# Optimization experiments

Hardware: AMD Instinct MI355X
Metric: run time of the kernel (lower is better)

## Reference

```python
import jax, jax.numpy as jnp
import numpy as np
from jax import lax

PC_RANGE = (-51.2, -51.2, -3.0, 51.2, 51.2, 1.0)
VOXEL = (0.4, 0.4, 4.0)
H = 256
W = 256
C = 256
EPS = 1e-5


def setup_inputs() -> dict:
    key = jax.random.key(0)
    ks = jax.random.split(key, 12)
    B, N = 4, 32
    # boxes: centers inside the BEV range with small corner offsets
    centers = jax.random.uniform(ks[0], (B, N, 1, 2), minval=-45.0, maxval=45.0)
    offsets = jax.random.normal(ks[1], (B, N, 8, 2)) * 2.0
    z = jax.random.normal(ks[2], (B, N, 8, 1))
    pred_box = jnp.concatenate([centers + offsets, z], axis=-1).astype(jnp.float32)
    pred_score = jax.random.uniform(ks[3], (B, N), dtype=jnp.float32)
    s = 0.02
    return {
        "pred_box": pred_box,
        "pred_score": pred_score,
        "W1": jax.random.normal(ks[4], (25, C), dtype=jnp.float32) * s,
        "b1": jnp.zeros((C,), jnp.float32),
        "W2": jax.random.normal(ks[5], (C, C), dtype=jnp.float32) * s,
        "b2": jnp.zeros((C,), jnp.float32),
        "W3": jax.random.normal(ks[6], (C, C), dtype=jnp.float32) * s,
        "b3": jnp.zeros((C,), jnp.float32),
        "conv_w": jax.random.normal(ks[7], (3, 2, C, C, 3, 3), dtype=jnp.float32) * s,
        "gamma": jnp.ones((3, 2, C), jnp.float32),
        "beta": jnp.zeros((3, 2, C), jnp.float32),
    }


def _conv(x, w):
    # x: [B,C,H,W], w: [O,I,3,3]
    return lax.conv_general_dilated(x, w, (1, 1), "SAME",
                                    dimension_numbers=("NCHW", "OIHW", "NCHW"))


def _bn(x, g, b):
    # BatchNorm2d in training mode; original runs with batch size 1 per CAV,
    # so stats are per-sample over (H,W). x: [B,C,H,W]
    m = x.mean(axis=(2, 3), keepdims=True)
    v = ((x - m) ** 2).mean(axis=(2, 3), keepdims=True)
    return (x - m) * jax.lax.rsqrt(v + EPS) * g[None, :, None, None] + b[None, :, None, None]


def reference(pred_box, pred_score, W1, b1, W2, b2, W3, b3, conv_w, gamma, beta):
    B, N = pred_box.shape[:2]
    xmin, ymin, _, xmax, ymax, _ = PC_RANGE
    dx, dy, _ = VOXEL

    # per-box MLP embedding
    geom = pred_box.reshape(B, N, 24)
    obj = jnp.concatenate([geom, pred_score[..., None]], axis=-1)  # [B,N,25]
    h1 = jax.nn.relu(obj @ W1 + b1)
    h2 = jax.nn.relu(h1 @ W2 + b2)
    obj_feat = (h2 @ W3 + b3) * pred_score[..., None]  # [B,N,C]

    # rasterize box AABBs onto the grid; later boxes overwrite earlier ones
    corners = pred_box[..., :2]  # [B,N,8,2]
    gx = jnp.floor((corners[..., 0] - xmin) / dx)
    gy = jnp.floor((corners[..., 1] - ymin) / dy)
    gx0 = jnp.clip(gx.min(-1), 0, W - 1).astype(jnp.int32)  # [B,N]
    gx1 = jnp.clip(gx.max(-1), 0, W - 1).astype(jnp.int32)
    gy0 = jnp.clip(gy.min(-1), 0, H - 1).astype(jnp.int32)
    gy1 = jnp.clip(gy.max(-1), 0, H - 1).astype(jnp.int32)

    xs = jnp.arange(W)
    ys = jnp.arange(H)
    mx = (xs[None, None, :] >= gx0[..., None]) & (xs[None, None, :] <= gx1[..., None])  # [B,N,W]
    my = (ys[None, None, :] >= gy0[..., None]) & (ys[None, None, :] <= gy1[..., None])  # [B,N,H]
    cover = my[:, :, :, None] & mx[:, :, None, :]  # [B,N,H,W]

    prio = jnp.arange(N, dtype=jnp.int32)[None, :, None, None]
    last = jnp.max(jnp.where(cover, prio, -1), axis=1)  # [B,H,W]: index of last covering box
    idx = jnp.clip(last, 0)
    gathered = jax.vmap(lambda of, ix: of[ix])(obj_feat, idx)  # [B,H,W,C]
    feat = jnp.where(last[..., None] >= 0, gathered, 0.0)
    x = jnp.transpose(feat, (0, 3, 1, 2))  # [B,C,H,W]

    # residual conv refine blocks
    for k in range(3):
        res = x
        y = jax.nn.relu(_bn(_conv(x, conv_w[k, 0]), gamma[k, 0], beta[k, 0]))
        y = _bn(_conv(y, conv_w[k, 1]), gamma[k, 1], beta[k, 1])
        x = jax.nn.relu(y + res)
    return x
```

## Files before the change

### kernel.cpp

```cpp
#include <hip/hip_runtime.h>
#include <hip/hip_bf16.h>

typedef short short8 __attribute__((ext_vector_type(8)));
typedef float f32x16 __attribute__((ext_vector_type(16)));

#define MFMA32 __builtin_amdgcn_mfma_f32_32x32x16_bf16
#define HWPX 65536

#define GLDS16(gp, lp) __builtin_amdgcn_global_load_lds( \
    (const __attribute__((address_space(1))) unsigned int*)(gp), \
    (__attribute__((address_space(3))) unsigned int*)(lp), 16, 0, 0)

__device__ __forceinline__ unsigned short f2bf(float f) {
  unsigned u = __float_as_uint(f);
  u += 0x7FFF + ((u >> 16) & 1);
  return (unsigned short)(u >> 16);
}
__device__ __forceinline__ float bf2f(unsigned short b) {
  return __uint_as_float(((unsigned)b) << 16);
}

__global__ void mlp_kernel(const float* __restrict__ pred_box,
                           const float* __restrict__ score,
                           const float* __restrict__ W1, const float* __restrict__ b1,
                           const float* __restrict__ W2, const float* __restrict__ b2,
                           const float* __restrict__ W3, const float* __restrict__ b3,
                           float* __restrict__ objf) {
  __shared__ float obj[25];
  __shared__ float h1[256];
  __shared__ float h2[256];
  const int box = blockIdx.x;
  const int tid = threadIdx.x;
  if (tid < 24) obj[tid] = pred_box[box * 24 + tid];
  if (tid == 24) obj[24] = score[box];
  __syncthreads();
  float acc = b1[tid];
  #pragma unroll
  for (int k = 0; k < 25; ++k) acc = fmaf(obj[k], W1[k * 256 + tid], acc);
  h1[tid] = fmaxf(acc, 0.f);
  __syncthreads();
  acc = b2[tid];
  #pragma unroll 8
  for (int k = 0; k < 256; ++k) acc = fmaf(h1[k], W2[k * 256 + tid], acc);
  h2[tid] = fmaxf(acc, 0.f);
  __syncthreads();
  acc = b3[tid];
  #pragma unroll 8
  for (int k = 0; k < 256; ++k) acc = fmaf(h2[k], W3[k * 256 + tid], acc);
  objf[box * 256 + tid] = acc * score[box];
}

__global__ void bounds_kernel(const float* __restrict__ pred_box,
                              int* __restrict__ bnds) {
  const int t = threadIdx.x;
  const float* p = pred_box + t * 24;
  float gx0 = 1e30f, gx1 = -1e30f, gy0 = 1e30f, gy1 = -1e30f;
  #pragma unroll
  for (int j = 0; j < 8; ++j) {
    float gx = floorf((p[j * 3 + 0] + 51.2f) / 0.4f);
    float gy = floorf((p[j * 3 + 1] + 51.2f) / 0.4f);
    gx0 = fminf(gx0, gx); gx1 = fmaxf(gx1, gx);
    gy0 = fminf(gy0, gy); gy1 = fmaxf(gy1, gy);
  }
  bnds[t * 4 + 0] = (int)fminf(fmaxf(gx0, 0.f), 255.f);
  bnds[t * 4 + 1] = (int)fminf(fmaxf(gx1, 0.f), 255.f);
  bnds[t * 4 + 2] = (int)fminf(fmaxf(gy0, 0.f), 255.f);
  bnds[t * 4 + 3] = (int)fminf(fmaxf(gy1, 0.f), 255.f);
}

__global__ void wt_kernel(const float* __restrict__ w, unsigned short* __restrict__ wt) {
  int i = blockIdx.x * 256 + threadIdx.x;
  int j = i & 7;
  int l = (i >> 3) & 63;
  int nb = (i >> 9) & 7;
  int ks = (i >> 12) & 15;
  int t2 = i >> 16;
  int tap = t2 % 9;
  int cv = t2 / 9;
  int co = nb * 32 + (l & 31);
  int ci = ks * 16 + ((l >> 5) << 3) + j;
  wt[i] = f2bf(w[(size_t)((cv * 256 + co) * 256 + ci) * 9 + tap]);
}

__global__ void raster_nhwc(const int* __restrict__ bnds,
                            const float* __restrict__ objf,
                            unsigned short* __restrict__ xB) {
  const int y = blockIdx.x;
  const int b = blockIdx.y;
  const int x = threadIdx.x;
  __shared__ int sb[128];
  __shared__ int lastA[256];
  if (x < 128) sb[x] = bnds[b * 128 + x];
  __syncthreads();
  int last = -1;
  #pragma unroll
  for (int n = 0; n < 32; ++n) {
    int bx0 = sb[n * 4 + 0], bx1 = sb[n * 4 + 1];
    int by0 = sb[n * 4 + 2], by1 = sb[n * 4 + 3];
    if (x >= bx0 && x <= bx1 && y >= by0 && y <= by1) last = n;
  }
  lastA[x] = last;
  __syncthreads();
  unsigned short* row = xB + ((size_t)b * HWPX + y * 256) * 256;
  for (int it = 0; it < 32; ++it) {
    int s = x + 256 * it;
    int px = s >> 5;
    int c8 = (s & 31) * 8;
    int ln = lastA[px];
    short8 v = {0, 0, 0, 0, 0, 0, 0, 0};
    if (ln >= 0) {
      const float* f = objf + (b * 32 + ln) * 256 + c8;
      #pragma unroll
      for (int j = 0; j < 8; ++j) v[j] = (short)f2bf(f[j]);
    }
    *(short8*)(row + px * 256 + c8) = v;
  }
}

__global__ __launch_bounds__(256, 2) void conv_mfma(const unsigned short* __restrict__ in,
                                                    const unsigned short* __restrict__ wt,
                                                    const unsigned short* __restrict__ zbuf,
                                                    unsigned short* __restrict__ T,
                                                    float* __restrict__ part) {
  __shared__ unsigned short lds[2][16 * 528];
  const int bid0 = blockIdx.x;
  const int swz = (bid0 & 7) * 256 + (bid0 >> 3);
  const int b = swz >> 9;
  const int bid = swz & 511;
  const int x0 = (bid & 3) * 64;
  const int y0 = (bid >> 2) * 2;
  const int tid = threadIdx.x;
  const int lane = tid & 63;
  const int wid = tid >> 6;
  const int h = lane >> 5;
  const int l31 = lane & 31;
  const int col0 = l31 * 8;

  const unsigned short* inb = in + (size_t)b * (HWPX * 256);
  unsigned short* Tb = T + (size_t)b * (HWPX * 256);

  f32x16 acc[4][2];
  #pragma unroll
  for (int a = 0; a < 4; ++a)
    #pragma unroll
    for (int n = 0; n < 2; ++n)
      #pragma unroll
      for (int r = 0; r < 16; ++r) acc[a][n][r] = 0.f;

  const unsigned short* wbase = wt + (size_t)(wid * 2) * 512 + lane * 8;

  short8 edgev;

  auto stage = [&](int c1, int buf) {
    const int ci0 = c1 * 32;
    #pragma unroll
    for (int i = 0; i < 4; ++i) {
      const int rowg = wid * 4 + i;
      const int row = rowg >> 2;
      const int g = rowg & 3;
      const int yg = y0 + row - 1;
      unsigned short* lp = &lds[buf][((row << 2) | ((g & 1) << 1) | (g >> 1)) * 528 + 8];
      const unsigned short* gp;
      if ((unsigned)yg < 256u)
        gp = inb + ((size_t)(yg * 256 + x0 + lane) * 256 + ci0 + g * 8);
      else
        gp = zbuf + lane * 8;
      GLDS16(gp, lp);
    }
  };

  auto edge_load = [&](int c1) {
    edgev = (short8){0, 0, 0, 0, 0, 0, 0, 0};
    if (tid < 32) {
      int row = tid >> 3, side = (tid >> 2) & 1, g = tid & 3;
      int yg = y0 + row - 1;
      int xg = x0 + (side ? 64 : -1);
      if ((unsigned)yg < 256u && (unsigned)xg < 256u)
        edgev = *(const short8*)(inb + ((size_t)(yg * 256 + xg) * 256 + c1 * 32 + g * 8));
    }
  };
  auto edge_store = [&](int buf) {
    if (tid < 32) {
      int row = tid >> 3, side = (tid >> 2) & 1, g = tid & 3;
      *(short8*)&lds[buf][((row << 2) | ((g & 1) << 1) | (g >> 1)) * 528 + (side ? 65 : 0) * 8] = edgev;
    }
  };

  #define LOADA(s, d) { \
    const int ks_ = (s) / 9, tap_ = (s) % 9, ky_ = tap_ / 3, kx_ = tap_ % 3; \
    const unsigned short* p_ = lbase + ky_ * 2112 + ks_ * 528 + kx_ * 8 + col0; \
    d[0] = *(const short8*)(p_); \
    d[1] = *(const short8*)(p_ + 256); \
    d[2] = *(const short8*)(p_ + 2112); \
    d[3] = *(const short8*)(p_ + 2368); }

  #define LOADB(s, d) { \
    const unsigned short* p_ = wbase + (size_t)((((s) % 9) * 16 + c * 2 + (s) / 9) * 8) * 512; \
    d[0] = *(const short8*)(p_); d[1] = *(const short8*)(p_ + 512); }

  auto compute = [&](int buf, int c) {
    const unsigned short* lbase = &lds[buf][h * 1056];
    short8 Af[2][4];
    short8 Bf[3][2];
    LOADA(0, Af[0]);
    LOADB(0, Bf[0]);
    LOADB(1, Bf[1]);
    #pragma unroll
    for (int s = 0; s < 18; ++s) {
      if (s + 2 < 18) LOADB(s + 2, Bf[(s + 2) % 3]);
      if (s + 1 < 18) LOADA(s + 1, Af[(s + 1) & 1]);
      __builtin_amdgcn_s_setprio(1);
      #pragma unroll
      for (int mf = 0; mf < 4; ++mf)
        #pragma unroll
        for (int nf = 0; nf < 2; ++nf)
          acc[mf][nf] = MFMA32(Af[s & 1][mf], Bf[s % 3][nf], acc[mf][nf], 0, 0, 0);
      __builtin_amdgcn_s_setprio(0);
    }
  };

  stage(0, 0);
  edge_load(0);
  edge_store(0);
  asm volatile("s_waitcnt lgkmcnt(0)" ::: "memory");

  int cur = 0;
  for (int c = 0; c < 8; ++c) {
    if (c < 7) {
      stage(c + 1, cur ^ 1);
      asm volatile("s_waitcnt vmcnt(8)" ::: "memory");
    } else {
      asm volatile("s_waitcnt vmcnt(0)" ::: "memory");
    }
    __builtin_amdgcn_s_barrier();
    if (c < 7) edge_load(c + 1);
    compute(cur, c);
    if (c < 7) edge_store(cur ^ 1);
    asm volatile("s_waitcnt lgkmcnt(0)" ::: "memory");
    __builtin_amdgcn_s_barrier();
    cur ^= 1;
  }

  #pragma unroll
  for (int mf = 0; mf < 4; ++mf)
    #pragma unroll
    for (int nf = 0; nf < 2; ++nf) {
      unsigned short* o = Tb + ((size_t)((y0 + (mf >> 1)) * 256) + x0 + (mf & 1) * 32) * 256
                          + wid * 64 + nf * 32 + l31;
      #pragma unroll
      for (int r = 0; r < 16; ++r) {
        int m = (r & 3) + 8 * (r >> 2) + 4 * h;
        o[(size_t)m * 256] = f2bf(acc[mf][nf][r]);
      }
    }
  #pragma unroll
  for (int nf = 0; nf < 2; ++nf) {
    float s = 0.f, s2 = 0.f;
    #pragma unroll
    for (int mf = 0; mf < 4; ++mf)
      #pragma unroll
      for (int r = 0; r < 16; ++r) {
        float v = acc[mf][nf][r];
        s += v; s2 += v * v;
      }
    s += __shfl_xor(s, 32);
    s2 += __shfl_xor(s2, 32);
    if (lane < 32) {
      part[((size_t)swz * 256 + wid * 64 + nf * 32 + lane) * 2] = s;
      part[((size_t)swz * 256 + wid * 64 + nf * 32 + lane) * 2 + 1] = s2;
    }
  }
  #undef LOADA
  #undef LOADB
}

__global__ void stats2(const float* __restrict__ part,
                       const float* __restrict__ g, const float* __restrict__ be,
                       float* __restrict__ sc, float* __restrict__ sh) {
  const int ch = blockIdx.x;
  const int b = blockIdx.y;
  const int t = threadIdx.x;
  double s = 0.0, s2 = 0.0;
  #pragma unroll
  for (int i = 0; i < 2; ++i) {
    int p = b * 512 + t + i * 256;
    s += (double)part[((size_t)p * 256 + ch) * 2];
    s2 += (double)part[((size_t)p * 256 + ch) * 2 + 1];
  }
  #pragma unroll
  for (int off = 32; off > 0; off >>= 1) {
    s += __shfl_down(s, off);
    s2 += __shfl_down(s2, off);
  }
  __shared__ double ls[4], ls2[4];
  if ((t & 63) == 0) { ls[t >> 6] = s; ls2[t >> 6] = s2; }
  __syncthreads();
  if (t == 0) {
    double S = ls[0] + ls[1] + ls[2] + ls[3];
    double S2 = ls2[0] + ls2[1] + ls2[2] + ls2[3];
    double m = S / 65536.0;
    double var = S2 / 65536.0 - m * m;
    double inv = 1.0 / sqrt(var + 1e-5);
    float scv = (float)inv * g[ch];
    sc[b * 256 + ch] = scv;
    sh[b * 256 + ch] = be[ch] - (float)m * scv;
  }
}

__global__ void bnrelu(const unsigned short* __restrict__ T,
                       const float* __restrict__ sc, const float* __restrict__ sh,
                       unsigned short* __restrict__ yB) {
  #pragma unroll
  for (int it = 0; it < 8; ++it) {
    size_t e = (size_t)it * 1048576 + blockIdx.x * 256 + threadIdx.x;
    int b = (int)(e >> 21);
    int ch8 = (int)(e & 31);
    const float* scp = sc + b * 256 + ch8 * 8;
    const float* shp = sh + b * 256 + ch8 * 8;
    float4 s0 = ((const float4*)scp)[0], s1 = ((const float4*)scp)[1];
    float4 h0 = ((const float4*)shp)[0], h1 = ((const float4*)shp)[1];
    float scv[8] = {s0.x, s0.y, s0.z, s0.w, s1.x, s1.y, s1.z, s1.w};
    float shv[8] = {h0.x, h0.y, h0.z, h0.w, h1.x, h1.y, h1.z, h1.w};
    short8 v = ((const short8*)T)[e];
    short8 o;
    #pragma unroll
    for (int j = 0; j < 8; ++j)
      o[j] = (short)f2bf(fmaxf(fmaf(bf2f((unsigned short)v[j]), scv[j], shv[j]), 0.f));
    ((short8*)yB)[e] = o;
  }
}

__global__ void bnres(const unsigned short* __restrict__ T,
                      const float* __restrict__ sc, const float* __restrict__ sh,
                      unsigned short* __restrict__ xB) {
  #pragma unroll
  for (int it = 0; it < 8; ++it) {
    size_t e = (size_t)it * 1048576 + blockIdx.x * 256 + threadIdx.x;
    int b = (int)(e >> 21);
    int ch8 = (int)(e & 31);
    const float* scp = sc + b * 256 + ch8 * 8;
    const float* shp = sh + b * 256 + ch8 * 8;
    float4 s0 = ((const float4*)scp)[0], s1 = ((const float4*)scp)[1];
    float4 h0 = ((const float4*)shp)[0], h1 = ((const float4*)shp)[1];
    float scv[8] = {s0.x, s0.y, s0.z, s0.w, s1.x, s1.y, s1.z, s1.w};
    float shv[8] = {h0.x, h0.y, h0.z, h0.w, h1.x, h1.y, h1.z, h1.w};
    short8 v = ((const short8*)T)[e];
    short8 rb = ((const short8*)xB)[e];
    short8 o;
    #pragma unroll
    for (int j = 0; j < 8; ++j) {
      float f = fmaf(bf2f((unsigned short)v[j]), scv[j], shv[j]) + bf2f((unsigned short)rb[j]);
      o[j] = (short)f2bf(fmaxf(f, 0.f));
    }
    ((short8*)xB)[e] = o;
  }
}

__global__ void bnres_tr(const unsigned short* __restrict__ T,
                         const float* __restrict__ sc, const float* __restrict__ sh,
                         const unsigned short* __restrict__ xB,
                         float* __restrict__ out) {
  __shared__ float tl[64][65];
  const int pxb = blockIdx.x >> 2;
  const int chb = blockIdx.x & 3;
  const int b = blockIdx.y;
  const int px0 = pxb * 64;
  const int ch0 = chb * 64;
  const int tid = threadIdx.x;
  #pragma unroll
  for (int i = 0; i < 2; ++i) {
    int p = (tid >> 3) + 32 * i;
    int c8 = (tid & 7) * 8;
    size_t e = ((size_t)b * HWPX + px0 + p) * 256 + ch0 + c8;
    const float* scp = sc + b * 256 + ch0 + c8;
    const float* shp = sh + b * 256 + ch0 + c8;
    float4 s0 = ((const float4*)scp)[0], s1 = ((const float4*)scp)[1];
    float4 h0 = ((const float4*)shp)[0], h1 = ((const float4*)shp)[1];
    float scv[8] = {s0.x, s0.y, s0.z, s0.w, s1.x, s1.y, s1.z, s1.w};
    float shv[8] = {h0.x, h0.y, h0.z, h0.w, h1.x, h1.y, h1.z, h1.w};
    short8 v = *(const short8*)(T + e);
    short8 rb = *(const short8*)(xB + e);
    #pragma unroll
    for (int j = 0; j < 8; ++j) {
      float f = fmaf(bf2f((unsigned short)v[j]), scv[j], shv[j]) + bf2f((unsigned short)rb[j]);
      tl[p][c8 + j] = fmaxf(f, 0.f);
    }
  }
  __syncthreads();
  float* ob = out + (size_t)b * (HWPX * 256);
  #pragma unroll
  for (int i = 0; i < 16; ++i) {
    int c = (tid >> 6) + 4 * i;
    int p = tid & 63;
    ob[(size_t)(ch0 + c) * HWPX + px0 + p] = tl[p][c];
  }
}

extern "C" void kernel_launch(void* const* d_in, const int* in_sizes, int n_in,
                              void* d_out, int out_size, void* d_ws, size_t ws_size,
                              hipStream_t stream) {
  const float* pred_box   = (const float*)d_in[0];
  const float* pred_score = (const float*)d_in[1];
  const float* W1 = (const float*)d_in[2];
  const float* b1 = (const float*)d_in[3];
  const float* W2 = (const float*)d_in[4];
  const float* b2 = (const float*)d_in[5];
  const float* W3 = (const float*)d_in[6];
  const float* b3 = (const float*)d_in[7];
  const float* conv_w = (const float*)d_in[8];
  const float* gamma  = (const float*)d_in[9];
  const float* beta   = (const float*)d_in[10];
  float* out = (float*)d_out;

  char* wsb = (char*)d_ws;
  float* objf = (float*)(wsb + 0);
  int*   bnds = (int*)(wsb + 0x40000);
  float* sc   = (float*)(wsb + 0x42000);
  float* sh   = (float*)(wsb + 0x44000);
  float* part = (float*)(wsb + 0x100000);
  unsigned short* zbuf = (unsigned short*)(wsb + 0x500000);
  unsigned short* wtAll = (unsigned short*)(wsb + 0x600000);
  unsigned short* xB = (unsigned short*)(wsb + (size_t)16 * 1024 * 1024);
  unsigned short* yB = (unsigned short*)(wsb + (size_t)160 * 1024 * 1024);
  unsigned short* T  = (unsigned short*)(wsb + (size_t)304 * 1024 * 1024);

  hipMemsetAsync(zbuf, 0, 4096, stream);
  mlp_kernel<<<128, 256, 0, stream>>>(pred_box, pred_score, W1, b1, W2, b2, W3, b3, objf);
  bounds_kernel<<<1, 128, 0, stream>>>(pred_box, bnds);
  wt_kernel<<<13824, 256, 0, stream>>>(conv_w, wtAll);
  raster_nhwc<<<dim3(256, 4), 256, 0, stream>>>(bnds, objf, xB);

  for (int k = 0; k < 3; ++k) {
    const unsigned short* wk0 = wtAll + (size_t)(k * 2 + 0) * 589824;
    const unsigned short* wk1 = wtAll + (size_t)(k * 2 + 1) * 589824;
    conv_mfma<<<2048, 256, 0, stream>>>(xB, wk0, zbuf, T, part);
    stats2<<<dim3(256, 4), 256, 0, stream>>>(part, gamma + (k * 2 + 0) * 256,
                                             beta + (k * 2 + 0) * 256, sc, sh);
    bnrelu<<<4096, 256, 0, stream>>>(T, sc, sh, yB);
    conv_mfma<<<2048, 256, 0, stream>>>(yB, wk1, zbuf, T, part);
    stats2<<<dim3(256, 4), 256, 0, stream>>>(part, gamma + (k * 2 + 1) * 256,
                                             beta + (k * 2 + 1) * 256, sc, sh);
    if (k < 2)
      bnres<<<4096, 256, 0, stream>>>(T, sc, sh, xB);
    else
      bnres_tr<<<dim3(4096, 4), 256, 0, stream>>>(T, sc, sh, xB, out);
  }
}
```

Measured before the change: 1.969 ms.

## Triple-buffer conv input staging and interleave loads into MFMA loop

The conv kernel's LDS input buffer goes from double to triple buffering. Each chunk's global-to-LDS loads are issued two iterations ahead and spread across the MFMA steps, and the next chunk's first weight fragments are prefetched at the end of the current chunk. This removes one of the two barriers per channel chunk and overlaps memory latency with compute. The cost is 50% more LDS per block, which may lower occupancy under the 2-blocks-per-CU launch bound. The manual vmcnt accounting is also more fragile.

```diff
diff --git a/kernel.cpp b/kernel.cpp
--- a/kernel.cpp
+++ b/kernel.cpp
@@ -122,7 +122,7 @@
                                                     const unsigned short* __restrict__ zbuf,
                                                     unsigned short* __restrict__ T,
                                                     float* __restrict__ part) {
-  __shared__ unsigned short lds[2][16 * 528];
+  __shared__ unsigned short lds[3][16 * 528];
   const int bid0 = blockIdx.x;
   const int swz = (bid0 & 7) * 256 + (bid0 >> 3);
   const int b = swz >> 9;
@@ -147,36 +147,33 @@
       #pragma unroll
       for (int r = 0; r < 16; ++r) acc[a][n][r] = 0.f;
 
+  short8 Af[2][4];
+  short8 Bf[3][2];
+  short8 edgev;
+
   const unsigned short* wbase = wt + (size_t)(wid * 2) * 512 + lane * 8;
 
-  short8 edgev;
-
-  auto stage = [&](int c1, int buf) {
-    const int ci0 = c1 * 32;
-    #pragma unroll
-    for (int i = 0; i < 4; ++i) {
-      const int rowg = wid * 4 + i;
-      const int row = rowg >> 2;
-      const int g = rowg & 3;
-      const int yg = y0 + row - 1;
-      unsigned short* lp = &lds[buf][((row << 2) | ((g & 1) << 1) | (g >> 1)) * 528 + 8];
-      const unsigned short* gp;
-      if ((unsigned)yg < 256u)
-        gp = inb + ((size_t)(yg * 256 + x0 + lane) * 256 + ci0 + g * 8);
-      else
-        gp = zbuf + lane * 8;
-      GLDS16(gp, lp);
-    }
+  auto stage1 = [&](int cc, int buf, int i) {
+    const int ci0 = cc * 32;
+    const int rowg = wid * 4 + i;
+    const int row = rowg >> 2;
+    const int g = rowg & 3;
+    const int yg = y0 + row - 1;
+    unsigned short* lp = &lds[buf][((row << 2) | ((g & 1) << 1) | (g >> 1)) * 528 + 8];
+    const unsigned short* gp = ((unsigned)yg < 256u)
+        ? inb + ((size_t)(yg * 256 + x0 + lane) * 256 + ci0 + g * 8)
+        : zbuf + lane * 8;
+    GLDS16(gp, lp);
   };
 
-  auto edge_load = [&](int c1) {
+  auto edge_load = [&](int cc) {
     edgev = (short8){0, 0, 0, 0, 0, 0, 0, 0};
     if (tid < 32) {
       int row = tid >> 3, side = (tid >> 2) & 1, g = tid & 3;
       int yg = y0 + row - 1;
       int xg = x0 + (side ? 64 : -1);
       if ((unsigned)yg < 256u && (unsigned)xg < 256u)
-        edgev = *(const short8*)(inb + ((size_t)(yg * 256 + xg) * 256 + c1 * 32 + g * 8));
+        edgev = *(const short8*)(inb + ((size_t)(yg * 256 + xg) * 256 + cc * 32 + g * 8));
     }
   };
   auto edge_store = [&](int buf) {
@@ -194,21 +191,34 @@
     d[2] = *(const short8*)(p_ + 2112); \
     d[3] = *(const short8*)(p_ + 2368); }
 
-  #define LOADB(s, d) { \
-    const unsigned short* p_ = wbase + (size_t)((((s) % 9) * 16 + c * 2 + (s) / 9) * 8) * 512; \
+  #define LOADBC(ccv, s, d) { \
+    const unsigned short* p_ = wbase + (size_t)((((s) % 9) * 16 + (ccv) * 2 + (s) / 9) * 8) * 512; \
     d[0] = *(const short8*)(p_); d[1] = *(const short8*)(p_ + 512); }
 
-  auto compute = [&](int buf, int c) {
-    const unsigned short* lbase = &lds[buf][h * 1056];
-    short8 Af[2][4];
-    short8 Bf[3][2];
+  edge_load(0);
+  #pragma unroll
+  for (int i = 0; i < 4; ++i) stage1(0, 0, i);
+  LOADBC(0, 0, Bf[0]);
+  LOADBC(0, 1, Bf[1]);
+  #pragma unroll
+  for (int i = 0; i < 4; ++i) stage1(1, 1, i);
+  edge_store(0);
+  asm volatile("s_waitcnt lgkmcnt(0)" ::: "memory");
+  asm volatile("s_waitcnt vmcnt(6)" ::: "memory");
+  __builtin_amdgcn_s_barrier();
+  __builtin_amdgcn_sched_barrier(0);
+
+  for (int c = 0; c < 8; ++c) {
+    if (c + 1 < 8) edge_load(c + 1);
+    const unsigned short* lbase = &lds[c % 3][0] + h * 1056;
     LOADA(0, Af[0]);
-    LOADB(0, Bf[0]);
-    LOADB(1, Bf[1]);
     #pragma unroll
     for (int s = 0; s < 18; ++s) {
-      if (s + 2 < 18) LOADB(s + 2, Bf[(s + 2) % 3]);
+      if (s + 2 < 18) { LOADBC(c, s + 2, Bf[(s + 2) % 3]); }
+      else if (c + 1 < 8) { LOADBC((c + 1), s + 2 - 18, Bf[(s + 2) % 3]); }
       if (s + 1 < 18) LOADA(s + 1, Af[(s + 1) & 1]);
+      if (c + 2 < 8 && (s == 4 || s == 6 || s == 8 || s == 10))
+        stage1(c + 2, (c + 2) % 3, (s - 4) >> 1);
       __builtin_amdgcn_s_setprio(1);
       #pragma unroll
       for (int mf = 0; mf < 4; ++mf)
@@ -217,28 +227,14 @@
           acc[mf][nf] = MFMA32(Af[s & 1][mf], Bf[s % 3][nf], acc[mf][nf], 0, 0, 0);
       __builtin_amdgcn_s_setprio(0);
     }
-  };
-
-  stage(0, 0);
-  edge_load(0);
-  edge_store(0);
-  asm volatile("s_waitcnt lgkmcnt(0)" ::: "memory");
-
-  int cur = 0;
-  for (int c = 0; c < 8; ++c) {
+    if (c + 1 < 8) edge_store((c + 1) % 3);
     if (c < 7) {
-      stage(c + 1, cur ^ 1);
-      asm volatile("s_waitcnt vmcnt(8)" ::: "memory");
-    } else {
-      asm volatile("s_waitcnt vmcnt(0)" ::: "memory");
-    }
-    __builtin_amdgcn_s_barrier();
-    if (c < 7) edge_load(c + 1);
-    compute(cur, c);
-    if (c < 7) edge_store(cur ^ 1);
-    asm volatile("s_waitcnt lgkmcnt(0)" ::: "memory");
-    __builtin_amdgcn_s_barrier();
-    cur ^= 1;
+      asm volatile("s_waitcnt lgkmcnt(0)" ::: "memory");
+      if (c == 6) { asm volatile("s_waitcnt vmcnt(2)" ::: "memory"); }
+      else        { asm volatile("s_waitcnt vmcnt(6)" ::: "memory"); }
+      __builtin_amdgcn_s_barrier();
+      __builtin_amdgcn_sched_barrier(0);
+    }
   }
 
   #pragma unroll
@@ -271,7 +267,7 @@
     }
   }
   #undef LOADA
-  #undef LOADB
+  #undef LOADBC
 }
 
 __global__ void stats2(const float* __restrict__ part,
```

Result: slower. 2.012 ms (+2.2%).
